# Optimization experiments

Measured on AMD Instinct MI355X. Metric: run time of the kernel, lower is better.

Reference implementation:

```python
import jax, jax.numpy as jnp
import numpy as np

N_EMBD = 768
HEAD_SIZE = 64

def setup_inputs() -> dict:
    key = jax.random.key(0)
    k1, k2, k3, k4 = jax.random.split(key, 4)
    B, T = 8, 2048
    x = jax.random.normal(k1, (B, T, N_EMBD), dtype=jnp.float32)
    s = 1.0 / np.sqrt(N_EMBD)
    Wk = jax.random.normal(k2, (N_EMBD, HEAD_SIZE), dtype=jnp.float32) * s
    Wq = jax.random.normal(k3, (N_EMBD, HEAD_SIZE), dtype=jnp.float32) * s
    Wv = jax.random.normal(k4, (N_EMBD, HEAD_SIZE), dtype=jnp.float32) * s
    return {"x": x, "Wk": Wk, "Wq": Wq, "Wv": Wv}

def reference(x, Wk, Wq, Wv):
    # x: [B, T, C]; projections: [B, T, H]
    B, T, C = x.shape
    k = jnp.einsum('btc,ch->bth', x, Wk)
    q = jnp.einsum('btc,ch->bth', x, Wq)
    v = jnp.einsum('btc,ch->bth', x, Wv)
    # scores [B, T, T], scaled by head_size^-0.5
    wei = jnp.einsum('bth,bsh->bts', q, k) * (HEAD_SIZE ** -0.5)
    causal = jnp.tril(jnp.ones((T, T), dtype=bool))
    wei = jnp.where(causal, wei, -jnp.inf)
    wei = jax.nn.softmax(wei, axis=-1)
    # dropout omitted (eval mode / deterministic reference)
    out = jnp.einsum('bts,bsh->bth', wei, v)
    return out
```

## Files before the change

kernel.cpp:

```cpp
#include <hip/hip_runtime.h>

#define B_ 8
#define T_ 2048
#define C_ 768
#define H_ 64
#define QT_ (T_ / 64)

typedef __bf16 bf16x8 __attribute__((ext_vector_type(8)));
typedef unsigned short ushort8 __attribute__((ext_vector_type(8)));
typedef float f32x4 __attribute__((ext_vector_type(4)));
typedef float f32x16 __attribute__((ext_vector_type(16)));

typedef __attribute__((address_space(1))) const void g_void;
typedef __attribute__((address_space(3))) void lds_void;

static __device__ __forceinline__ unsigned short f32_to_bf16(float f) {
  unsigned int u = __float_as_uint(f);
  u += 0x7FFFu + ((u >> 16) & 1u);
  return (unsigned short)(u >> 16);
}

static __device__ __forceinline__ unsigned int cvtpk_bf16(float a, float b) {
  unsigned int r;
  asm("v_cvt_pk_bf16_f32 %0, %1, %2" : "=v"(r) : "v"(a), "v"(b));
  return r;
}

static __device__ __forceinline__ f32x4 mfma16(ushort8 a, ushort8 b, f32x4 c) {
  return __builtin_amdgcn_mfma_f32_16x16x32_bf16(
      __builtin_bit_cast(bf16x8, a), __builtin_bit_cast(bf16x8, b), c, 0, 0, 0);
}

static __device__ __forceinline__ f32x16 mfma32(ushort8 a, ushort8 b, f32x16 c) {
  return __builtin_amdgcn_mfma_f32_32x32x16_bf16(
      __builtin_bit_cast(bf16x8, a), __builtin_bit_cast(bf16x8, b), c, 0, 0, 0);
}

template <int BASE>
static __device__ __forceinline__ ushort8 packA(const f32x16& p) {
  unsigned int a1 = cvtpk_bf16(p[BASE + 0], p[BASE + 1]);
  unsigned int a2 = cvtpk_bf16(p[BASE + 2], p[BASE + 3]);
  unsigned int a3 = cvtpk_bf16(p[BASE + 4], p[BASE + 5]);
  unsigned int a4 = cvtpk_bf16(p[BASE + 6], p[BASE + 7]);
  asm("v_permlane32_swap_b32 %0, %1" : "+v"(a1), "+v"(a3));
  asm("v_permlane32_swap_b32 %0, %1" : "+v"(a2), "+v"(a4));
  uint4 w = {a1, a2, a3, a4};
  return __builtin_bit_cast(ushort8, w);
}

__global__ void prep_w_kernel(const float* __restrict__ Wk, const float* __restrict__ Wq,
                              const float* __restrict__ Wv, unsigned short* __restrict__ Wt) {
  int g = blockIdx.x * 256 + threadIdx.x;
  if (g >= 24 * 768) return;
  int ks = g / 768, s = g - ks * 768;
  int n = s >> 2, perm = s & 3;
  int k8 = perm ^ (n & 3) ^ ((n >> 2) & 3);
  int p = n >> 6, col = n & 63;
  const float* W = (p == 0) ? Wk : (p == 1) ? Wq : Wv;
  float sc = (p == 1) ? 0.125f * 1.44269504088896f : 1.0f;
  int kbase = ks * 32 + k8 * 8;
  ushort8 v;
#pragma unroll
  for (int e = 0; e < 8; ++e) v[e] = f32_to_bf16(W[(kbase + e) * 64 + col] * sc);
  *(ushort8*)(Wt + (size_t)g * 8) = v;
}

__global__ __launch_bounds__(256) void proj_kernel(
    const float* __restrict__ x, const unsigned short* __restrict__ Wt,
    unsigned short* __restrict__ Qb, unsigned short* __restrict__ Kb,
    unsigned short* __restrict__ Vt) {
  __shared__ unsigned short Wl[2][6144];
  __shared__ unsigned short Xl[2][1024];
  const int tid = threadIdx.x;
  const int wave = tid >> 6, lane = tid & 63;
  const int lo = lane & 15, hi = lane >> 4;
  const int rg = wave & 1, ch2 = wave >> 1;
  const int row0 = blockIdx.x * 32;

  f32x4 acc[6];
#pragma unroll
  for (int t = 0; t < 6; ++t) acc[t] = (f32x4){0.f, 0.f, 0.f, 0.f};

  const int xr = (tid & 127) >> 2;
  const int xk8 = tid & 3;
  const int xslot = xr * 4 + (xk8 ^ (xr & 3) ^ ((xr >> 2) & 3));
  const float* xsrc = x + (size_t)(row0 + xr) * C_ + xk8 * 8;

  const int arow = rg * 16 + lo;
  const int aaddr = (arow * 4 + (hi ^ (arow & 3) ^ ((arow >> 2) & 3))) * 8;

  auto wstage = [&](int buf, int ks) {
    const unsigned short* src = Wt + (size_t)ks * 6144 + tid * 8;
#pragma unroll
    for (int is = 0; is < 3; ++is)
      __builtin_amdgcn_global_load_lds((g_void*)(src + is * 2048),
          (lds_void*)(&Wl[buf][is * 2048 + wave * 512]), 16, 0, 0);
  };

  float4 xa0 = {}, xa1 = {}, xb0 = {}, xb1 = {};

  wstage(0, 0);
  if (tid < 128) {
    xa0 = *(const float4*)(xsrc);
    xa1 = *(const float4*)(xsrc + 4);
  }

  for (int ks = 0; ks < 24; ++ks) {
    const int cur = ks & 1;
    asm volatile("s_waitcnt vmcnt(0)" ::: "memory");
    __syncthreads();
    if (ks + 1 < 24) {
      wstage(cur ^ 1, ks + 1);
      if (tid < 128) {
        xb0 = *(const float4*)(xsrc + (ks + 1) * 32);
        xb1 = *(const float4*)(xsrc + (ks + 1) * 32 + 4);
      }
    }
    if (tid < 128) {
      unsigned int dd[4];
      dd[0] = cvtpk_bf16(xa0.x, xa0.y);
      dd[1] = cvtpk_bf16(xa0.z, xa0.w);
      dd[2] = cvtpk_bf16(xa1.x, xa1.y);
      dd[3] = cvtpk_bf16(xa1.z, xa1.w);
      *(uint4*)(&Xl[cur][xslot * 8]) = *(uint4*)dd;
    }
    __syncthreads();
    ushort8 af = *(const ushort8*)(&Xl[cur][aaddr]);
#pragma unroll
    for (int t = 0; t < 6; ++t) {
      const int n = ch2 * 96 + t * 16 + lo;
      const int baddr = (n * 4 + (hi ^ (n & 3) ^ ((n >> 2) & 3))) * 8;
      ushort8 bfr = *(const ushort8*)(&Wl[cur][baddr]);
      acc[t] = mfma16(af, bfr, acc[t]);
    }
    xa0 = xb0; xa1 = xb1;
  }

#pragma unroll
  for (int t = 0; t < 6; ++t) {
    const int n = ch2 * 96 + t * 16 + lo;
    const int p = n >> 6, nn = n & 63;
#pragma unroll
    for (int r = 0; r < 4; ++r) {
      const int rgl = row0 + rg * 16 + hi * 4 + r;
      unsigned short val = f32_to_bf16(acc[t][r]);
      if (p == 0) {
        Kb[rgl * H_ + nn] = val;
      } else if (p == 1) {
        Qb[rgl * H_ + nn] = val;
      } else {
        const int b = rgl >> 11;
        const int tt = rgl & (T_ - 1);
        Vt[((b * H_ + nn) << 11) + tt] = val;
      }
    }
  }
}

__global__ __launch_bounds__(128) void attn_part_kernel(
    const unsigned short* __restrict__ Qb, const unsigned short* __restrict__ Kb,
    const unsigned short* __restrict__ Vt, float* __restrict__ Op, float* __restrict__ Ml,
    int chsz, int nch) {
  const int qt = blockIdx.x;
  const int b = blockIdx.y;
  const int ch = blockIdx.z;
  const int t0 = ch * chsz;
  if (t0 > qt) return;
  const int t1 = min(qt, t0 + chsz - 1);

  __shared__ __align__(16) unsigned short Kl[2][4096];
  __shared__ __align__(16) unsigned short Vl[2][4096];

  const int tid = threadIdx.x;
  const int wave = tid >> 6;
  const int lane = tid & 63;
  const int il = lane & 31;
  const int h = lane >> 5;
  const int i0w = qt * 64 + wave * 32;
  const size_t bt = (size_t)b * T_;

  const int srow = tid >> 3;
  const int sslot = (tid & 7) ^ (srow & 7);

  ushort8 qf[4];
#pragma unroll
  for (int dc = 0; dc < 4; ++dc)
    qf[dc] = *(const ushort8*)(Qb + (bt + i0w + il) * 64 + dc * 16 + h * 8);

  f32x16 o0 = {}, o1 = {};
  float m = -1e30f, lsum = 0.f;

  auto stage = [&](int buf, int jt) {
    const int j0 = jt * 64;
#pragma unroll
    for (int is = 0; is < 4; ++is) {
      const unsigned short* gK = Kb + ((bt + j0 + is * 16 + srow) << 6) + (sslot << 3);
      __builtin_amdgcn_global_load_lds((g_void*)gK,
          (lds_void*)(&Kl[buf][is * 1024 + wave * 512]), 16, 0, 0);
    }
#pragma unroll
    for (int is = 0; is < 4; ++is) {
      const unsigned short* gV = Vt + (((size_t)(b * H_ + is * 16 + srow)) << 11) + j0 + (sslot << 3);
      __builtin_amdgcn_global_load_lds((g_void*)gV,
          (lds_void*)(&Vl[buf][is * 1024 + wave * 512]), 16, 0, 0);
    }
  };

  stage(0, t0);

  for (int jt = t0; jt <= t1; ++jt) {
    const int cur = (jt - t0) & 1;
    asm volatile("s_waitcnt vmcnt(0)" ::: "memory");
    __syncthreads();
    if (jt < t1) stage(cur ^ 1, jt + 1);
    const int j0 = jt * 64;

    f32x16 s0 = {}, s1 = {};
    const unsigned short* KL = Kl[cur];
#pragma unroll
    for (int dc = 0; dc < 4; ++dc) {
      const int swz = ((dc * 2 + h) ^ (il & 7)) << 3;
      ushort8 k0 = *(const ushort8*)(&KL[(il << 6) + swz]);
      ushort8 k1 = *(const ushort8*)(&KL[((32 + il) << 6) + swz]);
      s0 = mfma32(k0, qf[dc], s0);
      s1 = mfma32(k1, qf[dc], s1);
    }

    if (jt == qt) {
      const int ig = i0w + il;
#pragma unroll
      for (int r = 0; r < 16; ++r) {
        const int jl = j0 + (r & 3) + 8 * (r >> 2) + 4 * h;
        if (jl > ig) s0[r] = -1e30f;
        if (jl + 32 > ig) s1[r] = -1e30f;
      }
    }

    float tm = s0[0];
#pragma unroll
    for (int r = 1; r < 16; ++r) tm = fmaxf(tm, s0[r]);
#pragma unroll
    for (int r = 0; r < 16; ++r) tm = fmaxf(tm, s1[r]);
    tm = fmaxf(tm, __shfl_xor(tm, 32));
    const float mnew = fmaxf(m, tm);
    const float scl = exp2f(m - mnew);
    m = mnew;
    float ts = 0.f;
#pragma unroll
    for (int r = 0; r < 16; ++r) { s0[r] = exp2f(s0[r] - mnew); ts += s0[r]; }
#pragma unroll
    for (int r = 0; r < 16; ++r) { s1[r] = exp2f(s1[r] - mnew); ts += s1[r]; }
    ts += __shfl_xor(ts, 32);
    lsum = lsum * scl + ts;
    o0 *= scl;
    o1 *= scl;

    const unsigned short* VL = Vl[cur];
#pragma unroll
    for (int c = 0; c < 4; ++c) {
      ushort8 pa = (c == 0) ? packA<0>(s0) : (c == 1) ? packA<8>(s0)
                 : (c == 2) ? packA<0>(s1) : packA<8>(s1);
      const int swz = ((c * 2 + h) ^ (il & 7)) << 3;
      ushort8 v0 = *(const ushort8*)(&VL[(il << 6) + swz]);
      ushort8 v1 = *(const ushort8*)(&VL[((32 + il) << 6) + swz]);
      o0 = mfma32(v0, pa, o0);
      o1 = mfma32(v1, pa, o1);
    }
  }

  const size_t pb = (size_t)(b * QT_ + qt) * nch + ch;
  float* op = Op + pb * 4096 + (size_t)(wave * 32 + il) * 64;
#pragma unroll
  for (int r = 0; r < 16; ++r) {
    const int dl = (r & 3) + 8 * (r >> 2) + 4 * h;
    op[dl] = o0[r];
    op[32 + dl] = o1[r];
  }
  if (h == 0) {
    float* ml = Ml + pb * 128;
    ml[wave * 32 + il] = m;
    ml[64 + wave * 32 + il] = lsum;
  }
}

__global__ __launch_bounds__(256) void attn_comb_kernel(
    const float* __restrict__ Op, const float* __restrict__ Ml, float* __restrict__ out,
    int chsz, int nch) {
  const int qt = blockIdx.x;
  const int b = blockIdx.y;
  const int nc = qt / chsz + 1;
  const int row = threadIdx.x >> 2;
  const int c0 = (threadIdx.x & 3) * 16;
  const size_t pbase = (size_t)(b * QT_ + qt) * nch;

  float m_g = -1e30f;
  for (int c = 0; c < nc; ++c) m_g = fmaxf(m_g, Ml[(pbase + c) * 128 + row]);
  float l_g = 0.f;
  for (int c = 0; c < nc; ++c)
    l_g += Ml[(pbase + c) * 128 + 64 + row] * exp2f(Ml[(pbase + c) * 128 + row] - m_g);
  const float inv = 1.0f / l_g;

  f32x4 a0 = {0,0,0,0}, a1 = {0,0,0,0}, a2 = {0,0,0,0}, a3 = {0,0,0,0};
  for (int c = 0; c < nc; ++c) {
    const float wc = exp2f(Ml[(pbase + c) * 128 + row] - m_g);
    const float* op = Op + (pbase + c) * 4096 + row * 64 + c0;
    a0 += *(const f32x4*)(op) * wc;
    a1 += *(const f32x4*)(op + 4) * wc;
    a2 += *(const f32x4*)(op + 8) * wc;
    a3 += *(const f32x4*)(op + 12) * wc;
  }
  float* o = out + ((size_t)b * T_ + qt * 64 + row) * 64 + c0;
  *(f32x4*)(o) = a0 * inv;
  *(f32x4*)(o + 4) = a1 * inv;
  *(f32x4*)(o + 8) = a2 * inv;
  *(f32x4*)(o + 12) = a3 * inv;
}

extern "C" void kernel_launch(void* const* d_in, const int* in_sizes, int n_in,
                              void* d_out, int out_size, void* d_ws, size_t ws_size,
                              hipStream_t stream) {
  const float* x = (const float*)d_in[0];
  const float* Wk = (const float*)d_in[1];
  const float* Wq = (const float*)d_in[2];
  const float* Wv = (const float*)d_in[3];
  float* out = (float*)d_out;

  char* ws = (char*)d_ws;
  unsigned short* Qb = (unsigned short*)(ws);
  unsigned short* Kb = (unsigned short*)(ws + (2u << 20));
  unsigned short* Vt = (unsigned short*)(ws + (4u << 20));
  unsigned short* Wt = (unsigned short*)(ws + (6u << 20));
  float* Op = (float*)(ws + (8u << 20));
  const size_t need8 = (8u << 20) + (size_t)8 * 4096 * B_ * QT_ * 4 + (size_t)8 * 128 * B_ * QT_ * 4;
  const int chsz = (ws_size >= need8) ? 4 : 8;
  const int nch = QT_ / chsz;
  float* Ml = (float*)(ws + (8u << 20) + (size_t)nch * 4096 * B_ * QT_ * 4);

  prep_w_kernel<<<dim3(72), dim3(256), 0, stream>>>(Wk, Wq, Wv, Wt);
  proj_kernel<<<dim3((B_ * T_) / 32), dim3(256), 0, stream>>>(x, Wt, Qb, Kb, Vt);
  attn_part_kernel<<<dim3(QT_, B_, nch), dim3(128), 0, stream>>>(Qb, Kb, Vt, Op, Ml, chsz, nch);
  attn_comb_kernel<<<dim3(QT_, B_), dim3(256), 0, stream>>>(Op, Ml, out, chsz, nch);
}
```

Baseline: 65.35 us.

## Load K/V MFMA fragments directly from global memory instead of LDS staging

Removes the double-buffered LDS staging of K and V tiles (global_load_lds plus waitcnt and barrier per tile). Each lane now loads its own K and V fragments straight from global memory into registers every iteration. This drops block-wide syncs and LDS traffic and frees LDS for occupancy. The cost is no cross-wave reuse through LDS, so both waves fetch the same K/V (relying on cache), and no explicit prefetch to hide load latency.

```diff
diff --git a/kernel.cpp b/kernel.cpp
--- a/kernel.cpp
+++ b/kernel.cpp
@@ -168,9 +168,6 @@
   if (t0 > qt) return;
   const int t1 = min(qt, t0 + chsz - 1);
 
-  __shared__ __align__(16) unsigned short Kl[2][4096];
-  __shared__ __align__(16) unsigned short Vl[2][4096];
-
   const int tid = threadIdx.x;
   const int wave = tid >> 6;
   const int lane = tid & 63;
@@ -179,51 +176,38 @@
   const int i0w = qt * 64 + wave * 32;
   const size_t bt = (size_t)b * T_;
 
-  const int srow = tid >> 3;
-  const int sslot = (tid & 7) ^ (srow & 7);
-
   ushort8 qf[4];
 #pragma unroll
   for (int dc = 0; dc < 4; ++dc)
     qf[dc] = *(const ushort8*)(Qb + (bt + i0w + il) * 64 + dc * 16 + h * 8);
 
+  const unsigned short* Kfr0 = Kb + ((bt + il) << 6) + h * 8;
+  const unsigned short* Vfr0 = Vt + (((size_t)(b * H_ + il)) << 11) + h * 8;
+
   f32x16 o0 = {}, o1 = {};
   float m = -1e30f, lsum = 0.f;
 
-  auto stage = [&](int buf, int jt) {
+  for (int jt = t0; jt <= t1; ++jt) {
     const int j0 = jt * 64;
-#pragma unroll
-    for (int is = 0; is < 4; ++is) {
-      const unsigned short* gK = Kb + ((bt + j0 + is * 16 + srow) << 6) + (sslot << 3);
-      __builtin_amdgcn_global_load_lds((g_void*)gK,
-          (lds_void*)(&Kl[buf][is * 1024 + wave * 512]), 16, 0, 0);
-    }
-#pragma unroll
-    for (int is = 0; is < 4; ++is) {
-      const unsigned short* gV = Vt + (((size_t)(b * H_ + is * 16 + srow)) << 11) + j0 + (sslot << 3);
-      __builtin_amdgcn_global_load_lds((g_void*)gV,
-          (lds_void*)(&Vl[buf][is * 1024 + wave * 512]), 16, 0, 0);
-    }
-  };
-
-  stage(0, t0);
-
-  for (int jt = t0; jt <= t1; ++jt) {
-    const int cur = (jt - t0) & 1;
-    asm volatile("s_waitcnt vmcnt(0)" ::: "memory");
-    __syncthreads();
-    if (jt < t1) stage(cur ^ 1, jt + 1);
-    const int j0 = jt * 64;
+
+    ushort8 kf0[4], kf1[4];
+#pragma unroll
+    for (int dc = 0; dc < 4; ++dc) {
+      kf0[dc] = *(const ushort8*)(Kfr0 + ((size_t)j0 << 6) + dc * 16);
+      kf1[dc] = *(const ushort8*)(Kfr0 + ((size_t)(j0 + 32) << 6) + dc * 16);
+    }
+    ushort8 vf0[4], vf1[4];
+#pragma unroll
+    for (int c = 0; c < 4; ++c) {
+      vf0[c] = *(const ushort8*)(Vfr0 + j0 + c * 16);
+      vf1[c] = *(const ushort8*)(Vfr0 + ((size_t)32 << 11) + j0 + c * 16);
+    }
 
     f32x16 s0 = {}, s1 = {};
-    const unsigned short* KL = Kl[cur];
 #pragma unroll
     for (int dc = 0; dc < 4; ++dc) {
-      const int swz = ((dc * 2 + h) ^ (il & 7)) << 3;
-      ushort8 k0 = *(const ushort8*)(&KL[(il << 6) + swz]);
-      ushort8 k1 = *(const ushort8*)(&KL[((32 + il) << 6) + swz]);
-      s0 = mfma32(k0, qf[dc], s0);
-      s1 = mfma32(k1, qf[dc], s1);
+      s0 = mfma32(kf0[dc], qf[dc], s0);
+      s1 = mfma32(kf1[dc], qf[dc], s1);
     }
 
     if (jt == qt) {
@@ -255,16 +239,12 @@
     o0 *= scl;
     o1 *= scl;
 
-    const unsigned short* VL = Vl[cur];
 #pragma unroll
     for (int c = 0; c < 4; ++c) {
       ushort8 pa = (c == 0) ? packA<0>(s0) : (c == 1) ? packA<8>(s0)
                  : (c == 2) ? packA<0>(s1) : packA<8>(s1);
-      const int swz = ((c * 2 + h) ^ (il & 7)) << 3;
-      ushort8 v0 = *(const ushort8*)(&VL[(il << 6) + swz]);
-      ushort8 v1 = *(const ushort8*)(&VL[((32 + il) << 6) + swz]);
-      o0 = mfma32(v0, pa, o0);
-      o1 = mfma32(v1, pa, o1);
+      o0 = mfma32(vf0[c], pa, o0);
+      o1 = mfma32(vf1[c], pa, o1);
     }
   }
 
```

Measured after the change: 76.00 us. +16.3%, slower.

## Split attention into 2-tile chunks with bf16 partials and no double buffering

Applied to the files above, without the earlier changes.

Fixes the split-KV chunk size at two key tiles (16 chunks per query tile), which multiplies the number of partial blocks to raise parallelism. It also drops LDS double buffering in favour of single-buffer load-then-compute, adds s_setprio around the MFMA sections, and stores the partial outputs as bf16 instead of fp32 to cut combine traffic. The cost is more blocks, more partial writes and reads, a longer combine loop, and precision lost on the partial outputs. The workspace layout is now hardcoded, with no size check.

```diff
diff --git a/kernel.cpp b/kernel.cpp
--- a/kernel.cpp
+++ b/kernel.cpp
@@ -5,6 +5,7 @@
 #define C_ 768
 #define H_ 64
 #define QT_ (T_ / 64)
+#define NCH_ 16
 
 typedef __bf16 bf16x8 __attribute__((ext_vector_type(8)));
 typedef unsigned short ushort8 __attribute__((ext_vector_type(8)));
@@ -18,6 +19,10 @@
   unsigned int u = __float_as_uint(f);
   u += 0x7FFFu + ((u >> 16) & 1u);
   return (unsigned short)(u >> 16);
+}
+
+static __device__ __forceinline__ float bf16_to_f32(unsigned short u) {
+  return __uint_as_float(((unsigned int)u) << 16);
 }
 
 static __device__ __forceinline__ unsigned int cvtpk_bf16(float a, float b) {
@@ -159,17 +164,17 @@
 
 __global__ __launch_bounds__(128) void attn_part_kernel(
     const unsigned short* __restrict__ Qb, const unsigned short* __restrict__ Kb,
-    const unsigned short* __restrict__ Vt, float* __restrict__ Op, float* __restrict__ Ml,
-    int chsz, int nch) {
+    const unsigned short* __restrict__ Vt, unsigned short* __restrict__ Opb,
+    float* __restrict__ Ml) {
   const int qt = blockIdx.x;
   const int b = blockIdx.y;
   const int ch = blockIdx.z;
-  const int t0 = ch * chsz;
+  const int t0 = ch * 2;
   if (t0 > qt) return;
-  const int t1 = min(qt, t0 + chsz - 1);
-
-  __shared__ __align__(16) unsigned short Kl[2][4096];
-  __shared__ __align__(16) unsigned short Vl[2][4096];
+  const int t1 = min(qt, t0 + 1);
+
+  __shared__ __align__(16) unsigned short Kl[4096];
+  __shared__ __align__(16) unsigned short Vl[4096];
 
   const int tid = threadIdx.x;
   const int wave = tid >> 6;
@@ -190,41 +195,40 @@
   f32x16 o0 = {}, o1 = {};
   float m = -1e30f, lsum = 0.f;
 
-  auto stage = [&](int buf, int jt) {
+  auto stage = [&](int jt) {
     const int j0 = jt * 64;
 #pragma unroll
     for (int is = 0; is < 4; ++is) {
       const unsigned short* gK = Kb + ((bt + j0 + is * 16 + srow) << 6) + (sslot << 3);
       __builtin_amdgcn_global_load_lds((g_void*)gK,
-          (lds_void*)(&Kl[buf][is * 1024 + wave * 512]), 16, 0, 0);
+          (lds_void*)(&Kl[is * 1024 + wave * 512]), 16, 0, 0);
     }
 #pragma unroll
     for (int is = 0; is < 4; ++is) {
       const unsigned short* gV = Vt + (((size_t)(b * H_ + is * 16 + srow)) << 11) + j0 + (sslot << 3);
       __builtin_amdgcn_global_load_lds((g_void*)gV,
-          (lds_void*)(&Vl[buf][is * 1024 + wave * 512]), 16, 0, 0);
+          (lds_void*)(&Vl[is * 1024 + wave * 512]), 16, 0, 0);
     }
   };
 
-  stage(0, t0);
-
   for (int jt = t0; jt <= t1; ++jt) {
-    const int cur = (jt - t0) & 1;
+    if (jt > t0) __syncthreads();
+    stage(jt);
     asm volatile("s_waitcnt vmcnt(0)" ::: "memory");
     __syncthreads();
-    if (jt < t1) stage(cur ^ 1, jt + 1);
     const int j0 = jt * 64;
 
     f32x16 s0 = {}, s1 = {};
-    const unsigned short* KL = Kl[cur];
+    __builtin_amdgcn_s_setprio(1);
 #pragma unroll
     for (int dc = 0; dc < 4; ++dc) {
       const int swz = ((dc * 2 + h) ^ (il & 7)) << 3;
-      ushort8 k0 = *(const ushort8*)(&KL[(il << 6) + swz]);
-      ushort8 k1 = *(const ushort8*)(&KL[((32 + il) << 6) + swz]);
+      ushort8 k0 = *(const ushort8*)(&Kl[(il << 6) + swz]);
+      ushort8 k1 = *(const ushort8*)(&Kl[((32 + il) << 6) + swz]);
       s0 = mfma32(k0, qf[dc], s0);
       s1 = mfma32(k1, qf[dc], s1);
     }
+    __builtin_amdgcn_s_setprio(0);
 
     if (jt == qt) {
       const int ig = i0w + il;
@@ -255,26 +259,31 @@
     o0 *= scl;
     o1 *= scl;
 
-    const unsigned short* VL = Vl[cur];
+    __builtin_amdgcn_s_setprio(1);
 #pragma unroll
     for (int c = 0; c < 4; ++c) {
       ushort8 pa = (c == 0) ? packA<0>(s0) : (c == 1) ? packA<8>(s0)
                  : (c == 2) ? packA<0>(s1) : packA<8>(s1);
       const int swz = ((c * 2 + h) ^ (il & 7)) << 3;
-      ushort8 v0 = *(const ushort8*)(&VL[(il << 6) + swz]);
-      ushort8 v1 = *(const ushort8*)(&VL[((32 + il) << 6) + swz]);
+      ushort8 v0 = *(const ushort8*)(&Vl[(il << 6) + swz]);
+      ushort8 v1 = *(const ushort8*)(&Vl[((32 + il) << 6) + swz]);
       o0 = mfma32(v0, pa, o0);
       o1 = mfma32(v1, pa, o1);
     }
-  }
-
-  const size_t pb = (size_t)(b * QT_ + qt) * nch + ch;
-  float* op = Op + pb * 4096 + (size_t)(wave * 32 + il) * 64;
-#pragma unroll
-  for (int r = 0; r < 16; ++r) {
-    const int dl = (r & 3) + 8 * (r >> 2) + 4 * h;
-    op[dl] = o0[r];
-    op[32 + dl] = o1[r];
+    __builtin_amdgcn_s_setprio(0);
+  }
+
+  const size_t pb = (size_t)(b * QT_ + qt) * NCH_ + ch;
+  unsigned short* op = Opb + pb * 4096 + (size_t)(wave * 32 + il) * 64;
+#pragma unroll
+  for (int g = 0; g < 4; ++g) {
+    unsigned int w0[2], w1[2];
+    w0[0] = cvtpk_bf16(o0[4 * g + 0], o0[4 * g + 1]);
+    w0[1] = cvtpk_bf16(o0[4 * g + 2], o0[4 * g + 3]);
+    w1[0] = cvtpk_bf16(o1[4 * g + 0], o1[4 * g + 1]);
+    w1[1] = cvtpk_bf16(o1[4 * g + 2], o1[4 * g + 3]);
+    *(uint2*)(op + 8 * g + 4 * h) = *(uint2*)w0;
+    *(uint2*)(op + 32 + 8 * g + 4 * h) = *(uint2*)w1;
   }
   if (h == 0) {
     float* ml = Ml + pb * 128;
@@ -284,14 +293,14 @@
 }
 
 __global__ __launch_bounds__(256) void attn_comb_kernel(
-    const float* __restrict__ Op, const float* __restrict__ Ml, float* __restrict__ out,
-    int chsz, int nch) {
+    const unsigned short* __restrict__ Opb, const float* __restrict__ Ml,
+    float* __restrict__ out) {
   const int qt = blockIdx.x;
   const int b = blockIdx.y;
-  const int nc = qt / chsz + 1;
+  const int nc = (qt >> 1) + 1;
   const int row = threadIdx.x >> 2;
   const int c0 = (threadIdx.x & 3) * 16;
-  const size_t pbase = (size_t)(b * QT_ + qt) * nch;
+  const size_t pbase = (size_t)(b * QT_ + qt) * NCH_;
 
   float m_g = -1e30f;
   for (int c = 0; c < nc; ++c) m_g = fmaxf(m_g, Ml[(pbase + c) * 128 + row]);
@@ -303,11 +312,13 @@
   f32x4 a0 = {0,0,0,0}, a1 = {0,0,0,0}, a2 = {0,0,0,0}, a3 = {0,0,0,0};
   for (int c = 0; c < nc; ++c) {
     const float wc = exp2f(Ml[(pbase + c) * 128 + row] - m_g);
-    const float* op = Op + (pbase + c) * 4096 + row * 64 + c0;
-    a0 += *(const f32x4*)(op) * wc;
-    a1 += *(const f32x4*)(op + 4) * wc;
-    a2 += *(const f32x4*)(op + 8) * wc;
-    a3 += *(const f32x4*)(op + 12) * wc;
+    const unsigned short* op = Opb + (pbase + c) * 4096 + row * 64 + c0;
+    ushort8 u0 = *(const ushort8*)(op);
+    ushort8 u1 = *(const ushort8*)(op + 8);
+    a0 += (f32x4){bf16_to_f32(u0[0]), bf16_to_f32(u0[1]), bf16_to_f32(u0[2]), bf16_to_f32(u0[3])} * wc;
+    a1 += (f32x4){bf16_to_f32(u0[4]), bf16_to_f32(u0[5]), bf16_to_f32(u0[6]), bf16_to_f32(u0[7])} * wc;
+    a2 += (f32x4){bf16_to_f32(u1[0]), bf16_to_f32(u1[1]), bf16_to_f32(u1[2]), bf16_to_f32(u1[3])} * wc;
+    a3 += (f32x4){bf16_to_f32(u1[4]), bf16_to_f32(u1[5]), bf16_to_f32(u1[6]), bf16_to_f32(u1[7])} * wc;
   }
   float* o = out + ((size_t)b * T_ + qt * 64 + row) * 64 + c0;
   *(f32x4*)(o) = a0 * inv;
@@ -330,14 +341,11 @@
   unsigned short* Kb = (unsigned short*)(ws + (2u << 20));
   unsigned short* Vt = (unsigned short*)(ws + (4u << 20));
   unsigned short* Wt = (unsigned short*)(ws + (6u << 20));
-  float* Op = (float*)(ws + (8u << 20));
-  const size_t need8 = (8u << 20) + (size_t)8 * 4096 * B_ * QT_ * 4 + (size_t)8 * 128 * B_ * QT_ * 4;
-  const int chsz = (ws_size >= need8) ? 4 : 8;
-  const int nch = QT_ / chsz;
-  float* Ml = (float*)(ws + (8u << 20) + (size_t)nch * 4096 * B_ * QT_ * 4);
+  unsigned short* Opb = (unsigned short*)(ws + (8u << 20));
+  float* Ml = (float*)(ws + (40u << 20));
 
   prep_w_kernel<<<dim3(72), dim3(256), 0, stream>>>(Wk, Wq, Wv, Wt);
   proj_kernel<<<dim3((B_ * T_) / 32), dim3(256), 0, stream>>>(x, Wt, Qb, Kb, Vt);
-  attn_part_kernel<<<dim3(QT_, B_, nch), dim3(128), 0, stream>>>(Qb, Kb, Vt, Op, Ml, chsz, nch);
-  attn_comb_kernel<<<dim3(QT_, B_), dim3(256), 0, stream>>>(Op, Ml, out, chsz, nch);
-}
+  attn_part_kernel<<<dim3(QT_, B_, NCH_), dim3(128), 0, stream>>>(Qb, Kb, Vt, Opb, Ml);
+  attn_comb_kernel<<<dim3(QT_, B_), dim3(256), 0, stream>>>(Opb, Ml, out);
+}
```

Measured after the change: 74.92 us. 1.15x slower.
